# Performance work log

Hardware: AMD Instinct MI355X
Metric: run time of the kernel (lower is better)

Reference implementation:

```python
import jax, jax.numpy as jnp
import numpy as np

D_MODEL = 512
N_HEADS = 8
HEAD_DIM = D_MODEL // N_HEADS          # 64
ROTARY_DIM = HEAD_DIM // 2             # 32 (rotary_frac = 0.5)
MAX_SEQ_LEN = 512
EPS = 1e-6


def _rope_tables(seq_len, dtype=jnp.float32):
    inv_freq = 1.0 / (10000.0 ** (jnp.arange(0, ROTARY_DIM, 2, dtype=jnp.float32) / ROTARY_DIM))
    t = jnp.arange(seq_len, dtype=jnp.float32)
    freqs = jnp.outer(t, inv_freq)          # (T, ROTARY_DIM//2)
    return jnp.sin(freqs).astype(dtype), jnp.cos(freqs).astype(dtype)


def _apply_rope(x, sin, cos):
    # x: (R, H, T, Dh); rotate interleaved pairs of the first ROTARY_DIM dims
    rd = ROTARY_DIM
    x1 = x[..., :rd].reshape(*x.shape[:-1], rd // 2, 2)
    x2 = x[..., rd:]
    s = sin[None, None, :, :]
    c = cos[None, None, :, :]
    a, b = x1[..., 0], x1[..., 1]
    rot = jnp.stack([a * c - b * s, a * s + b * c], axis=-1).reshape(*x.shape[:-1], rd)
    return jnp.concatenate([rot, x2], axis=-1)


def setup_inputs() -> dict:
    key = jax.random.key(0)
    ks = jax.random.split(key, 8)
    B, T, N, D = 1, 384, 128, D_MODEL
    x = jax.random.normal(ks[0], (B, T, N, D), dtype=jnp.float32)
    neuron_pad_mask = jax.random.randint(ks[1], (B, N), 0, 2, dtype=jnp.int32)
    scale = 1.0 / np.sqrt(D)
    norm_w = jnp.ones((D,), dtype=jnp.float32)
    wq = jax.random.normal(ks[2], (D, D), dtype=jnp.float32) * scale
    wk = jax.random.normal(ks[3], (D, D), dtype=jnp.float32) * scale
    wv = jax.random.normal(ks[4], (D, D), dtype=jnp.float32) * scale
    wo = jax.random.normal(ks[5], (D, D), dtype=jnp.float32) * scale
    return {"x": x, "neuron_pad_mask": neuron_pad_mask, "norm_w": norm_w,
            "wq": wq, "wk": wk, "wv": wv, "wo": wo}


def reference(x, neuron_pad_mask, norm_w, wq, wk, wv, wo):
    B, T, N, D = x.shape
    H, Dh = N_HEADS, HEAD_DIM

    # RMSNorm over d_model
    xn = x * jax.lax.rsqrt(jnp.mean(x * x, axis=-1, keepdims=True) + EPS) * norm_w

    # (B,T,N,D) -> (B*N, T, D): each neuron is an independent causal timeline
    xt = jnp.transpose(xn, (0, 2, 1, 3)).reshape(B * N, T, D)
    res = xt

    # QKV projections (Linear, no bias: x @ W^T), split into heads -> (R,H,T,Dh)
    def to_bhld(y):
        return jnp.transpose(y.reshape(B * N, T, H, Dh), (0, 2, 1, 3))

    q = to_bhld(xt @ wq.T)
    k = to_bhld(xt @ wk.T)
    v = to_bhld(xt @ wv.T)

    sin, cos = _rope_tables(T, dtype=x.dtype)
    q = _apply_rope(q, sin, cos)
    k = _apply_rope(k, sin, cos)

    # Causal SDPA per row (scale = 1/sqrt(Dh), matching F.scaled_dot_product_attention)
    scores = jnp.einsum('rhtd,rhsd->rhts', q, k) / np.sqrt(Dh).astype(x.dtype)
    causal = jnp.tril(jnp.ones((T, T), dtype=bool))
    scores = jnp.where(causal[None, None], scores, jnp.finfo(scores.dtype).min)
    attn = jax.nn.softmax(scores, axis=-1)
    out = jnp.einsum('rhts,rhsd->rhtd', attn, v)            # (R,H,T,Dh)
    out = jnp.transpose(out, (0, 2, 1, 3)).reshape(B * N, T, D)

    # Only valid (non-padded) neuron rows receive attention output (others stay 0)
    valid = (neuron_pad_mask.reshape(-1) != 0)
    out = jnp.where(valid[:, None, None], out, jnp.zeros((), dtype=out.dtype))

    out = out + res
    out = jnp.transpose(out.reshape(B, N, T, D), (0, 2, 1, 3))  # (B,T,N,D)
    return out @ wo.T
```

## Files before the change

### kernel.cpp

```cpp
#include <hip/hip_runtime.h>
#include <hip/hip_bf16.h>
#include <stdint.h>

typedef __bf16 bf16x8 __attribute__((ext_vector_type(8)));
typedef float f32x4 __attribute__((ext_vector_type(4)));

static constexpr int T_SEQ  = 384;
static constexpr int NNEUR  = 128;
static constexpr int DMODEL = 512;
static constexpr int NROWS  = NNEUR * T_SEQ;
static constexpr float ROPE_C = 0.8304820237218406f;

__device__ __forceinline__ float bf2f(unsigned short u) {
  union { unsigned int i; float f; } x; x.i = ((unsigned int)u) << 16; return x.f;
}
__device__ __forceinline__ unsigned short f2bf(float f) {
  union { float f; unsigned int i; } x; x.f = f;
  unsigned int i = x.i;
  i += 0x7FFFu + ((i >> 16) & 1u);
  return (unsigned short)(i >> 16);
}
__device__ __forceinline__ float fast_exp2(float x) {
#if __has_builtin(__builtin_amdgcn_exp2f)
  return __builtin_amdgcn_exp2f(x);
#else
  return exp2f(x);
#endif
}

__device__ __forceinline__ void async_copy16(const unsigned short* g, unsigned short* l) {
  auto gp = reinterpret_cast<const __attribute__((address_space(1))) unsigned int*>(
      reinterpret_cast<uintptr_t>(g));
  auto lp = reinterpret_cast<__attribute__((address_space(3))) unsigned int*>(
      reinterpret_cast<uintptr_t>(l));
  __builtin_amdgcn_global_load_lds(gp, lp, 16, 0, 0);
}

__global__ __launch_bounds__(256) void prep_kernel(
    const float* __restrict__ w0, const float* __restrict__ w1,
    const float* __restrict__ w2, const float* __restrict__ w3,
    unsigned short* __restrict__ o0, unsigned short* __restrict__ o1,
    unsigned short* __restrict__ o2, unsigned short* __restrict__ o3,
    float2* __restrict__ tab)
{
  if (blockIdx.y == 4) {
    if (blockIdx.x >= 24) return;
    int idx = blockIdx.x * 256 + threadIdx.x;
    int t = idx >> 4, i = idx & 15;
    float ang = (float)t * exp2f(-(float)i * ROPE_C);
    float s, c; sincosf(ang, &s, &c);
    tab[idx] = make_float2(s, c);
    return;
  }
  const float* w; unsigned short* o;
  switch (blockIdx.y) {
    case 0:  w = w0; o = o0; break;
    case 1:  w = w1; o = o1; break;
    case 2:  w = w2; o = o2; break;
    default: w = w3; o = o3; break;
  }
  int i = (blockIdx.x * 256 + threadIdx.x) * 4;
  float4 v = *reinterpret_cast<const float4*>(w + i);
  union { unsigned short u[4]; uint2 v2; } p;
  p.u[0] = f2bf(v.x); p.u[1] = f2bf(v.y); p.u[2] = f2bf(v.z); p.u[3] = f2bf(v.w);
  *reinterpret_cast<uint2*>(o + i) = p.v2;
}

__global__ __launch_bounds__(256) void rmsnorm_kernel(
    const float* __restrict__ x, const float* __restrict__ nw,
    unsigned short* __restrict__ xt)
{
  int wave = threadIdx.x >> 6, lane = threadIdx.x & 63;
  int rid = blockIdx.x * 4 + wave;
  int t = rid >> 7, n = rid & 127;
  const float* row = x + (size_t)rid * DMODEL;
  float4 v0 = *reinterpret_cast<const float4*>(row + lane * 8);
  float4 v1 = *reinterpret_cast<const float4*>(row + lane * 8 + 4);
  float ss = v0.x*v0.x + v0.y*v0.y + v0.z*v0.z + v0.w*v0.w
           + v1.x*v1.x + v1.y*v1.y + v1.z*v1.z + v1.w*v1.w;
  #pragma unroll
  for (int off = 32; off; off >>= 1) ss += __shfl_xor(ss, off);
  float sc = rsqrtf(ss * (1.0f / DMODEL) + 1e-6f);
  float4 w0 = *reinterpret_cast<const float4*>(nw + lane * 8);
  float4 w1 = *reinterpret_cast<const float4*>(nw + lane * 8 + 4);
  union { unsigned short u[8]; uint4 v; } p;
  p.u[0] = f2bf(v0.x * sc * w0.x); p.u[1] = f2bf(v0.y * sc * w0.y);
  p.u[2] = f2bf(v0.z * sc * w0.z); p.u[3] = f2bf(v0.w * sc * w0.w);
  p.u[4] = f2bf(v1.x * sc * w1.x); p.u[5] = f2bf(v1.y * sc * w1.y);
  p.u[6] = f2bf(v1.z * sc * w1.z); p.u[7] = f2bf(v1.w * sc * w1.w);
  *reinterpret_cast<uint4*>(xt + ((size_t)n * T_SEQ + t) * DMODEL + lane * 8) = p.v;
}

template <int MODE, typename OutT>
__global__ __launch_bounds__(256, 4) void gemm_k(
    const unsigned short* __restrict__ A,
    const unsigned short* __restrict__ B,
    OutT* __restrict__ C,
    const float2* __restrict__ tab,
    const int* __restrict__ pad)
{
  __shared__ alignas(16) unsigned short Sh[256 * 64];
  const int tid  = threadIdx.x;
  const int wave = tid >> 6, lane = tid & 63;
  const int l15  = lane & 15, quad = lane >> 4;
  const int wm = (wave >> 1) * 64, wn = (wave & 1) * 64;

  constexpr int GX = (MODE == 2) ? 8 : 4;
  constexpr int GY = 384;
  constexpr int NB = GX * GY;
  constexpr int CH = NB / 8;
  const int lin = (int)blockIdx.y * GX + (int)blockIdx.x;
  const int swz = (lin & 7) * CH + (lin >> 3);
  const int bx  = swz % GX, by = swz / GX;

  size_t m0; int n0;
  if constexpr (MODE == 3) { m0 = (size_t)bx * 128; n0 = by * 128; }
  else                     { m0 = (size_t)by * 128; n0 = bx * 128; }

  if constexpr (MODE == 2) {
    if (pad[(int)(m0 / 384)] == 0) return;
  }
  if constexpr (MODE == 3) {
    if (pad[n0 / 384] == 0) return;
  }

  const int r0 = tid >> 3;
  const int gc = (tid & 7) ^ (r0 & 7);
  const unsigned short* ga = A + (m0 + r0) * 512 + gc * 8;
  const unsigned short* gb = B + ((size_t)n0 + r0) * 512 + gc * 8;
  unsigned short* ls = &Sh[tid * 8];

  f32x4 acc[4][4] = {};
  for (int k0 = 0; k0 < 512; k0 += 64) {
    #pragma unroll
    for (int rr = 0; rr < 4; ++rr) {
      async_copy16(ga + (size_t)rr * 32 * 512 + k0, ls + rr * 2048);
      async_copy16(gb + (size_t)rr * 32 * 512 + k0, ls + 8192 + rr * 2048);
    }
    __syncthreads();
    #pragma unroll
    for (int kc = 0; kc < 2; ++kc) {
      const int pc = ((kc * 4 + quad) ^ (l15 & 7)) * 8;
      bf16x8 a[4], b[4];
      #pragma unroll
      for (int i = 0; i < 4; ++i)
        a[i] = *reinterpret_cast<const bf16x8*>(&Sh[(wm + i * 16 + l15) * 64 + pc]);
      #pragma unroll
      for (int j = 0; j < 4; ++j)
        b[j] = *reinterpret_cast<const bf16x8*>(&Sh[(128 + wn + j * 16 + l15) * 64 + pc]);
      #pragma unroll
      for (int i = 0; i < 4; ++i)
        #pragma unroll
        for (int j = 0; j < 4; ++j)
          acc[i][j] = __builtin_amdgcn_mfma_f32_16x16x32_bf16(a[i], b[j], acc[i][j], 0, 0, 0);
    }
    __syncthreads();
  }

  if constexpr (MODE == 3) {
    #pragma unroll
    for (int j = 0; j < 4; ++j) {
      int xbase = n0 + wn + j * 16;
      int nn    = xbase / 384;
      int bloc  = xbase - nn * 384;
      int off64 = (bloc >> 6) * 64 + ((bloc >> 4) & 3);
      #pragma unroll
      for (int i = 0; i < 4; ++i)
        #pragma unroll
        for (int r = 0; r < 4; ++r) {
          int dout = (int)m0 + wm + i * 16 + quad * 4 + r;
          C[((size_t)nn * 512 + dout) * 384 + off64 + l15 * 4] = f2bf(acc[i][j][r]);
        }
    }
  } else {
    OutT* Cb = C;
    int ncol0 = n0 + wn;
    if constexpr (MODE == 2) {
      int sec = n0 >> 9;
      Cb = C + (size_t)sec * NROWS * 512;
      ncol0 = (n0 & 511) + wn;
    }
    #pragma unroll
    for (int i = 0; i < 4; ++i) {
      #pragma unroll
      for (int r = 0; r < 4; ++r) {
        size_t grow = m0 + wm + i * 16 + quad * 4 + r;
        int t = (int)(grow % 384);
        #pragma unroll
        for (int j = 0; j < 4; ++j) {
          float v = acc[i][j][r];
          int col = ncol0 + j * 16 + l15;
          if constexpr (MODE == 2) {
            if (((ncol0 + j * 16) & 63) < 32) {
              float part = __shfl_xor(v, 1);
              float2 scv = tab[t * 16 + ((col & 63) >> 1)];
              v = (l15 & 1) ? (part * scv.x + v * scv.y)
                            : (v * scv.y - part * scv.x);
            }
            Cb[grow * 512 + col] = f2bf(v);
          } else {
            Cb[grow * 512 + col] = v;
          }
        }
      }
    }
  }
}

__global__ __launch_bounds__(256, 4) void attn_kernel(
    const unsigned short* __restrict__ qb,
    const unsigned short* __restrict__ kb,
    const unsigned short* __restrict__ vt,
    const unsigned short* __restrict__ xt,
    const int* __restrict__ pad,
    unsigned short* __restrict__ y)
{
  const int lin = (int)blockIdx.x + 3 * ((int)blockIdx.y + 8 * (int)blockIdx.z);
  const int swz = (lin & 7) * 384 + (lin >> 3);
  const int qtb = swz % 3;
  const int rem = swz / 3;
  const int h   = rem & 7;
  const int n   = rem >> 3;

  const int tid  = threadIdx.x;

  if (pad[n] == 0) {
    int rb = tid >> 2;
    int d  = h * 64 + (tid & 3) * 16;
    #pragma unroll
    for (int rr = 0; rr < 128; rr += 64) {
      int tq = qtb * 128 + rr + rb;
      const uint4* src = reinterpret_cast<const uint4*>(
          &xt[((size_t)n * T_SEQ + tq) * 512 + d]);
      uint4* dst = reinterpret_cast<uint4*>(
          &y[((size_t)tq * NNEUR + n) * 512 + d]);
      dst[0] = src[0];
      dst[1] = src[1];
    }
    return;
  }

  __shared__ alignas(16) unsigned short Qs[128 * 64];
  __shared__ alignas(16) unsigned short Ks[64 * 64];
  __shared__ alignas(16) unsigned short VTs[64 * 64];
  __shared__ alignas(16) unsigned short Ps[4][16][72];

  const int wave = tid >> 6, lane = tid & 63;
  const int l15  = lane & 15, quad = lane >> 4;
  const int lrow = lane >> 3, lchunk = (lane & 7) ^ ((lane >> 3) & 7);
  const float C2 = 0.18033688011112042f;

  const unsigned short* gq =
      qb + ((size_t)n * T_SEQ + qtb * 128 + wave * 32 + lrow) * 512 + h * 64 + lchunk * 8;
  #pragma unroll
  for (int rr = 0; rr < 4; ++rr)
    async_copy16(gq + (size_t)(rr * 8) * 512, &Qs[(wave * 32 + rr * 8) * 64]);

  const unsigned short* gk0 =
      kb + ((size_t)n * T_SEQ + wave * 16 + lrow) * 512 + h * 64 + lchunk * 8;
  const unsigned short* gv0 =
      vt + ((size_t)n * 512 + h * 64 + wave * 16 + lrow) * 384 + lchunk * 8;

  const int nkt = 2 * qtb + 2;

  float lsum[2][4] = {};
  f32x4 oacc[2][4] = {};

  async_copy16(gk0,           &Ks[(wave * 16) * 64]);
  async_copy16(gk0 + 8 * 512, &Ks[(wave * 16 + 8) * 64]);
  async_copy16(gv0,           &VTs[(wave * 16) * 64]);
  async_copy16(gv0 + 8 * 384, &VTs[(wave * 16 + 8) * 64]);
  __syncthreads();

  bf16x8 aq[2][2];
  #pragma unroll
  for (int s = 0; s < 2; ++s)
    #pragma unroll
    for (int kc = 0; kc < 2; ++kc) {
      const int pcq = ((kc * 4 + quad) ^ (l15 & 7)) * 8;
      aq[s][kc] = *reinterpret_cast<const bf16x8*>(
          &Qs[(wave * 32 + s * 16 + l15) * 64 + pcq]);
    }

  for (int kt = 0; kt < nkt; ++kt) {
    #pragma unroll
    for (int s = 0; s < 2; ++s) {
      const int qsub = qtb * 128 + wave * 32 + s * 16;
      if (kt * 64 > qsub + 15) continue;

      f32x4 sc4[4] = {};
      #pragma unroll
      for (int kc = 0; kc < 2; ++kc) {
        const int pc = ((kc * 4 + quad) ^ (l15 & 7)) * 8;
        #pragma unroll
        for (int tc = 0; tc < 4; ++tc) {
          bf16x8 bk = *reinterpret_cast<const bf16x8*>(&Ks[(tc * 16 + l15) * 64 + pc]);
          sc4[tc] = __builtin_amdgcn_mfma_f32_16x16x32_bf16(aq[s][kc], bk, sc4[tc], 0, 0, 0);
        }
      }
      float ps_[4][4];
      #pragma unroll
      for (int tc = 0; tc < 4; ++tc)
        #pragma unroll
        for (int r = 0; r < 4; ++r) {
          float p = fast_exp2(sc4[tc][r] * C2 - 16.0f);
          int kglob = kt * 64 + tc * 16 + l15;
          int qglob = qsub + quad * 4 + r;
          if (kglob > qglob) p = 0.f;
          lsum[s][r] += p;
          ps_[tc][r] = p;
        }
      #pragma unroll
      for (int r = 0; r < 4; ++r) {
        union { float f; unsigned int u; } a0, a1, a2, a3;
        a0.f = ps_[0][r]; a1.f = ps_[1][r]; a2.f = ps_[2][r]; a3.f = ps_[3][r];
        uint2 pk;
        pk.x = (a1.u & 0xffff0000u) | (a0.u >> 16);
        pk.y = (a3.u & 0xffff0000u) | (a2.u >> 16);
        *reinterpret_cast<uint2*>(&Ps[wave][quad * 4 + r][l15 * 4]) = pk;
      }
      #pragma unroll
      for (int kc = 0; kc < 2; ++kc) {
        const int pc = ((kc * 4 + quad) ^ (l15 & 7)) * 8;
        bf16x8 ap = *reinterpret_cast<const bf16x8*>(&Ps[wave][l15][kc * 32 + quad * 8]);
        #pragma unroll
        for (int dt = 0; dt < 4; ++dt) {
          bf16x8 bv = *reinterpret_cast<const bf16x8*>(&VTs[(dt * 16 + l15) * 64 + pc]);
          oacc[s][dt] = __builtin_amdgcn_mfma_f32_16x16x32_bf16(ap, bv, oacc[s][dt], 0, 0, 0);
        }
      }
    }
    if (kt + 1 < nkt) {
      __syncthreads();
      const size_t ko = (size_t)(kt + 1) * 64;
      async_copy16(gk0 + ko * 512,                 &Ks[(wave * 16) * 64]);
      async_copy16(gk0 + (ko + 8) * 512,           &Ks[(wave * 16 + 8) * 64]);
      async_copy16(gv0 + (kt + 1) * 64,            &VTs[(wave * 16) * 64]);
      async_copy16(gv0 + (kt + 1) * 64 + 8 * 384,  &VTs[(wave * 16 + 8) * 64]);
      __syncthreads();
    }
  }

  float inv[2][4];
  #pragma unroll
  for (int s = 0; s < 2; ++s)
    #pragma unroll
    for (int r = 0; r < 4; ++r) {
      float l = lsum[s][r];
      l += __shfl_xor(l, 1);
      l += __shfl_xor(l, 2);
      l += __shfl_xor(l, 4);
      l += __shfl_xor(l, 8);
      inv[s][r] = 1.0f / l;
    }
  #pragma unroll
  for (int s = 0; s < 2; ++s)
    #pragma unroll
    for (int dt = 0; dt < 4; ++dt)
      #pragma unroll
      for (int r = 0; r < 4; ++r) {
        int tq = qtb * 128 + wave * 32 + s * 16 + quad * 4 + r;
        int d  = h * 64 + dt * 16 + l15;
        float val = oacc[s][dt][r] * inv[s][r];
        float res = bf2f(xt[((size_t)n * T_SEQ + tq) * 512 + d]);
        y[((size_t)tq * NNEUR + n) * 512 + d] = f2bf(val + res);
      }
}

extern "C" void kernel_launch(void* const* d_in, const int* in_sizes, int n_in,
                              void* d_out, int out_size, void* d_ws, size_t ws_size,
                              hipStream_t stream) {
  const float* x   = (const float*)d_in[0];
  const int*   pad = (const int*)d_in[1];
  const float* nw  = (const float*)d_in[2];
  const float* wq  = (const float*)d_in[3];
  const float* wk  = (const float*)d_in[4];
  const float* wv  = (const float*)d_in[5];
  const float* wo  = (const float*)d_in[6];
  float* out = (float*)d_out;

  char* ws = (char*)d_ws;
  size_t off = 0;
  auto alloc = [&](size_t bytes) { void* p = ws + off; off += (bytes + 255) & ~(size_t)255; return p; };
  const size_t WELEM  = (size_t)512 * 512;
  const size_t MBYTES = (size_t)NROWS * 512 * 2;
  unsigned short* wqkv_bf = (unsigned short*)alloc(WELEM * 3 * 2);
  unsigned short* wo_bf   = (unsigned short*)alloc(WELEM * 2);
  float2*         rtab    = (float2*)alloc(384 * 16 * sizeof(float2));
  unsigned short* xt_bf   = (unsigned short*)alloc(MBYTES);
  unsigned short* qk_buf  = (unsigned short*)alloc(MBYTES * 2);
  unsigned short* vt_buf  = (unsigned short*)alloc(MBYTES);
  unsigned short* y_buf   = (unsigned short*)alloc(MBYTES);

  prep_kernel<<<dim3(256, 5), 256, 0, stream>>>(
      wq, wk, wv, wo,
      wqkv_bf, wqkv_bf + WELEM, wqkv_bf + 2 * WELEM, wo_bf, rtab);
  rmsnorm_kernel<<<NROWS / 4, 256, 0, stream>>>(x, nw, xt_bf);
  gemm_k<2, unsigned short><<<dim3(8, NROWS / 128), 256, 0, stream>>>(
      xt_bf, wqkv_bf, qk_buf, rtab, pad);
  gemm_k<3, unsigned short><<<dim3(4, NROWS / 128), 256, 0, stream>>>(
      wqkv_bf + 2 * WELEM, xt_bf, vt_buf, nullptr, pad);
  attn_kernel<<<dim3(3, 8, 128), 256, 0, stream>>>(
      qk_buf, qk_buf + (size_t)NROWS * 512, vt_buf, xt_bf, pad, y_buf);
  gemm_k<0, float><<<dim3(4, NROWS / 128), 256, 0, stream>>>(
      y_buf, wo_bf, out, nullptr, pad);
}
```

Measured before the change: 342.0 us.

## Triple-buffer GEMM K-loop with async prefetch and MFMA priority boost

Replaces the single-buffered 64-wide K loop in the projection GEMMs with a 3-stage ring of 32-wide K tiles. Global-to-LDS async copies for tile t+2 are issued while tile t is computed, using explicit vmcnt waits and raw barriers in place of full syncthreads. It also raises wave priority around the MFMA block and lowers the launch-bounds occupancy hint from 4 to 3 blocks per CU. The aim is to hide global load latency behind matrix math, at the cost of more LDS per block and possibly lower occupancy.

```diff
diff --git a/kernel.cpp b/kernel.cpp
--- a/kernel.cpp
+++ b/kernel.cpp
@@ -92,14 +92,14 @@
 }
 
 template <int MODE, typename OutT>
-__global__ __launch_bounds__(256, 4) void gemm_k(
+__global__ __launch_bounds__(256, 3) void gemm_k(
     const unsigned short* __restrict__ A,
     const unsigned short* __restrict__ B,
     OutT* __restrict__ C,
     const float2* __restrict__ tab,
     const int* __restrict__ pad)
 {
-  __shared__ alignas(16) unsigned short Sh[256 * 64];
+  __shared__ alignas(16) unsigned short Sh[3][8192];
   const int tid  = threadIdx.x;
   const int wave = tid >> 6, lane = tid & 63;
   const int l15  = lane & 15, quad = lane >> 4;
@@ -124,38 +124,58 @@
     if (pad[n0 / 384] == 0) return;
   }
 
-  const int r0 = tid >> 3;
-  const int gc = (tid & 7) ^ (r0 & 7);
-  const unsigned short* ga = A + (m0 + r0) * 512 + gc * 8;
-  const unsigned short* gb = B + ((size_t)n0 + r0) * 512 + gc * 8;
-  unsigned short* ls = &Sh[tid * 8];
+  const int r = tid >> 2;
+  const int gc = (tid & 3) ^ (r & 3);
+  const unsigned short* ga = A + (m0 + r) * 512 + gc * 8;
+  const unsigned short* gb = B + ((size_t)n0 + r) * 512 + gc * 8;
+
+  const int pc = (quad ^ (l15 & 3)) * 8;
+
+  auto STAGE = [&](int kk, int b) {
+    const unsigned short* gak = ga + kk * 32;
+    const unsigned short* gbk = gb + kk * 32;
+    unsigned short* base = &Sh[b][0] + tid * 8;
+    async_copy16(gak,            base);
+    async_copy16(gak + 64 * 512, base + 2048);
+    async_copy16(gbk,            base + 4096);
+    async_copy16(gbk + 64 * 512, base + 4096 + 2048);
+  };
 
   f32x4 acc[4][4] = {};
-  for (int k0 = 0; k0 < 512; k0 += 64) {
-    #pragma unroll
-    for (int rr = 0; rr < 4; ++rr) {
-      async_copy16(ga + (size_t)rr * 32 * 512 + k0, ls + rr * 2048);
-      async_copy16(gb + (size_t)rr * 32 * 512 + k0, ls + 8192 + rr * 2048);
-    }
-    __syncthreads();
-    #pragma unroll
-    for (int kc = 0; kc < 2; ++kc) {
-      const int pc = ((kc * 4 + quad) ^ (l15 & 7)) * 8;
-      bf16x8 a[4], b[4];
-      #pragma unroll
-      for (int i = 0; i < 4; ++i)
-        a[i] = *reinterpret_cast<const bf16x8*>(&Sh[(wm + i * 16 + l15) * 64 + pc]);
+  auto COMPUTE = [&](int b) {
+    const unsigned short* base = &Sh[b][0];
+    bf16x8 a[4], bb[4];
+    #pragma unroll
+    for (int i = 0; i < 4; ++i)
+      a[i] = *reinterpret_cast<const bf16x8*>(&base[(wm + i * 16 + l15) * 32 + pc]);
+    #pragma unroll
+    for (int j = 0; j < 4; ++j)
+      bb[j] = *reinterpret_cast<const bf16x8*>(&base[4096 + (wn + j * 16 + l15) * 32 + pc]);
+    __builtin_amdgcn_s_setprio(1);
+    #pragma unroll
+    for (int i = 0; i < 4; ++i)
       #pragma unroll
       for (int j = 0; j < 4; ++j)
-        b[j] = *reinterpret_cast<const bf16x8*>(&Sh[(128 + wn + j * 16 + l15) * 64 + pc]);
-      #pragma unroll
-      for (int i = 0; i < 4; ++i)
-        #pragma unroll
-        for (int j = 0; j < 4; ++j)
-          acc[i][j] = __builtin_amdgcn_mfma_f32_16x16x32_bf16(a[i], b[j], acc[i][j], 0, 0, 0);
-    }
-    __syncthreads();
-  }
+        acc[i][j] = __builtin_amdgcn_mfma_f32_16x16x32_bf16(a[i], bb[j], acc[i][j], 0, 0, 0);
+    __builtin_amdgcn_s_setprio(0);
+  };
+
+  STAGE(0, 0);
+  STAGE(1, 1);
+  #pragma unroll
+  for (int t = 0; t < 14; ++t) {
+    STAGE(t + 2, (t + 2) % 3);
+    asm volatile("s_waitcnt vmcnt(8)" ::: "memory");
+    __builtin_amdgcn_s_barrier();
+    COMPUTE(t % 3);
+    __builtin_amdgcn_s_barrier();
+  }
+  asm volatile("s_waitcnt vmcnt(4)" ::: "memory");
+  __builtin_amdgcn_s_barrier();
+  COMPUTE(14 % 3);
+  asm volatile("s_waitcnt vmcnt(0)" ::: "memory");
+  __builtin_amdgcn_s_barrier();
+  COMPUTE(15 % 3);
 
   if constexpr (MODE == 3) {
     #pragma unroll
@@ -167,9 +187,9 @@
       #pragma unroll
       for (int i = 0; i < 4; ++i)
         #pragma unroll
-        for (int r = 0; r < 4; ++r) {
-          int dout = (int)m0 + wm + i * 16 + quad * 4 + r;
-          C[((size_t)nn * 512 + dout) * 384 + off64 + l15 * 4] = f2bf(acc[i][j][r]);
+        for (int r2 = 0; r2 < 4; ++r2) {
+          int dout = (int)m0 + wm + i * 16 + quad * 4 + r2;
+          C[((size_t)nn * 512 + dout) * 384 + off64 + l15 * 4] = f2bf(acc[i][j][r2]);
         }
     }
   } else {
@@ -183,12 +203,12 @@
     #pragma unroll
     for (int i = 0; i < 4; ++i) {
       #pragma unroll
-      for (int r = 0; r < 4; ++r) {
-        size_t grow = m0 + wm + i * 16 + quad * 4 + r;
+      for (int r2 = 0; r2 < 4; ++r2) {
+        size_t grow = m0 + wm + i * 16 + quad * 4 + r2;
         int t = (int)(grow % 384);
         #pragma unroll
         for (int j = 0; j < 4; ++j) {
-          float v = acc[i][j][r];
+          float v = acc[i][j][r2];
           int col = ncol0 + j * 16 + l15;
           if constexpr (MODE == 2) {
             if (((ncol0 + j * 16) & 63) < 32) {
```

Result: no change. 338.7 us (-1.0%).
